# Performance work log

Measured on AMD Instinct MI355X. Metric: run time of the kernel, lower is better.

The kernel has to match this reference:

```python
import jax, jax.numpy as jnp
import numpy as np
from jax import lax

PAD_TOKEN = 1
VOCAB = 32000
HID = 512
B, T, M = 32, 512, 6


def setup_inputs() -> dict:
    key = jax.random.key(0)
    ks = jax.random.split(key, 12)
    lim_g = 1.0 / np.sqrt(HID)
    lim_w = 1.0 / np.sqrt(2 * HID)
    u = lambda k, shape, lim: jax.random.uniform(k, shape, jnp.float32, -lim, lim)
    inp = {
        "input_seqs": jax.random.randint(ks[0], (B, T, M), 0, VOCAB, dtype=jnp.int32),
        "input_lengths": jax.random.randint(ks[1], (B,), 1, T + 1, dtype=jnp.int32),
        "emb": jax.random.normal(ks[2], (VOCAB, HID), jnp.float32),
        # forward GRU cell (Keras GRUCell, reset_after=True)
        "k_f": u(ks[3], (HID, 3 * HID), lim_g),
        "rk_f": u(ks[4], (HID, 3 * HID), lim_g),
        "b_f": u(ks[5], (2, 3 * HID), lim_g),
        # backward GRU cell
        "k_b": u(ks[6], (HID, 3 * HID), lim_g),
        "rk_b": u(ks[7], (HID, 3 * HID), lim_g),
        "b_b": u(ks[8], (2, 3 * HID), lim_g),
        # output projection W: 2H -> H
        "Wk": u(ks[9], (2 * HID, HID), lim_w),
        "Wb": u(ks[10], (HID,), lim_w),
    }
    return inp


def _gru_dir(x, mask, kernel, rkernel, bias, reverse):
    """Masked GRU scan. x: [B,T,H], mask: [B,T] bool. Keras GRUCell (reset_after=True).
    Masked timesteps carry previous state/output through (Keras semantics)."""
    b_in, b_rec = bias[0], bias[1]
    xs = x @ kernel + b_in                      # [B,T,3H], precompute input GEMM
    xs_t = jnp.swapaxes(xs, 0, 1)               # [T,B,3H]
    m_t = jnp.swapaxes(mask, 0, 1)              # [T,B]
    h0 = jnp.zeros((x.shape[0], rkernel.shape[0]), x.dtype)

    def step(h, inp):
        xt, mt = inp
        inner = h @ rkernel + b_rec             # [B,3H]
        xz, xr, xh = jnp.split(xt, 3, axis=-1)
        iz, ir, ih = jnp.split(inner, 3, axis=-1)
        z = jax.nn.sigmoid(xz + iz)
        r = jax.nn.sigmoid(xr + ir)
        hh = jnp.tanh(xh + r * ih)
        hn = z * h + (1.0 - z) * hh
        hn = jnp.where(mt[:, None], hn, h)      # masked step: carry state
        return hn, hn

    hT, outs = lax.scan(step, h0, (xs_t, m_t), reverse=reverse)
    return jnp.swapaxes(outs, 0, 1), hT         # [B,T,H], [B,H]


def reference(input_seqs, input_lengths, emb, k_f, rk_f, b_f, k_b, rk_b, b_b, Wk, Wb):
    # embedding lookup + PAD masking, sum over memory-tuple axis
    e = emb[input_seqs]                                       # [B,T,M,H]
    pad_mask = (input_seqs != PAD_TOKEN).astype(e.dtype)      # [B,T,M]
    embedded = jnp.sum(e * pad_mask[..., None], axis=2)       # [B,T,H]
    # (dropout p=0.0 -> identity)

    time_mask = jnp.arange(T)[None, :] < input_lengths[:, None]  # [B,T] bool

    out_f, h_f = _gru_dir(embedded, time_mask, k_f, rk_f, b_f, reverse=False)
    out_b, h_b = _gru_dir(embedded, time_mask, k_b, rk_b, b_b, reverse=True)

    outputs = jnp.concatenate([out_f, out_b], axis=-1)        # [B,T,2H]
    hidden_hat = jnp.concatenate([h_f, h_b], axis=-1)         # [B,2H]

    hidden = hidden_hat @ Wk + Wb                             # [B,H]
    outputs = outputs @ Wk + Wb                               # [B,T,H]
    return outputs, hidden
```

## Files before the change

kernel.cpp:

```cpp
#include <hip/hip_runtime.h>

typedef _Float16 f16;
typedef f16  f16x8 __attribute__((ext_vector_type(8)));
typedef float f32x4 __attribute__((ext_vector_type(4)));
typedef unsigned int u32;
typedef unsigned long long u64;
typedef u32 u32x4 __attribute__((ext_vector_type(4)));

#define NB   32
#define NT   512
#define NM   6
#define NH   512
#define NH3  1536
#define PADTOK 1
#define LO_SCALE 4096.0f
#define LO_INV   (1.0f/4096.0f)

#define FLAGS_OFF 168165376
#define FLAGS_U32 (2 * (NT + 1) * 32)

__global__ __launch_bounds__(128) void k_embed(const int* __restrict__ seqs,
                                               const float* __restrict__ emb,
                                               f16* __restrict__ Ahi,
                                               f16* __restrict__ Alo,
                                               f16* __restrict__ A2,
                                               u32* __restrict__ flags) {
  int row = blockIdx.x;
  int tid = threadIdx.x;
  if (row < 32) {
    for (int c2 = tid; c2 < 1024; c2 += 128)
      A2[(size_t)(16416 + row) * 1024 + c2] = (f16)0.f;
  }
  if (row < 64) {
    for (int j = row * 128 + tid; j < FLAGS_U32; j += 64 * 128)
      flags[j] = 0u;
  }
  const int* tr = seqs + (size_t)row * NM;
  int c0 = tid * 4;
  float acc0 = 0.f, acc1 = 0.f, acc2 = 0.f, acc3 = 0.f;
  for (int m = 0; m < NM; m++) {
    int tk = tr[m];
    if (tk != PADTOK) {
      float4 ev = *(const float4*)(emb + (size_t)tk * NH + c0);
      acc0 += ev.x; acc1 += ev.y; acc2 += ev.z; acc3 += ev.w;
    }
  }
  float a[4] = {acc0, acc1, acc2, acc3};
  for (int j = 0; j < 4; j++) {
    float v = a[j];
    f16 h = (f16)v;
    float lo = (v - (float)h) * LO_SCALE;
    Ahi[(size_t)row * NH + c0 + j] = h;
    Alo[(size_t)row * NH + c0 + j] = (f16)lo;
  }
}

__global__ __launch_bounds__(256) void k_gemm_in(const f16* __restrict__ Ahi,
                                                 const f16* __restrict__ Alo,
                                                 const float* __restrict__ Bw,
                                                 const float* __restrict__ bias,
                                                 f16* __restrict__ Cxs,
                                                 f16* __restrict__ Clo) {
  __shared__ f16 BsH[64][40];
  __shared__ f16 BsL[64][40];
  int bx = blockIdx.x, by = blockIdx.y;
  int tid = threadIdx.x;
  int w = tid >> 6, l = tid & 63;
  int row0 = bx * 64 + w * 16;
  int col0 = by * 64;
  int arow = row0 + (l & 15);
  int kg = (l >> 4) * 8;
  f32x4 acc[4], accs[4];
  for (int nt = 0; nt < 4; nt++) {
    float bv = bias[col0 + nt * 16 + (l & 15)];
    f32x4 t = {bv, bv, bv, bv};
    acc[nt] = t;
    f32x4 z = {0.f, 0.f, 0.f, 0.f};
    accs[nt] = z;
  }
  for (int kb = 0; kb < NH; kb += 32) {
    __syncthreads();
    for (int idx = tid; idx < 2048; idx += 256) {
      int n = idx & 63, kl = idx >> 6;
      float v = Bw[(size_t)(kb + kl) * NH3 + col0 + n];
      f16 h = (f16)v;
      BsH[n][kl] = h;
      BsL[n][kl] = (f16)((v - (float)h) * LO_SCALE);
    }
    __syncthreads();
    f16x8 ah = *(const f16x8*)(Ahi + (size_t)arow * NH + kb + kg);
    f16x8 al = *(const f16x8*)(Alo + (size_t)arow * NH + kb + kg);
    for (int nt = 0; nt < 4; nt++) {
      f16x8 bh = *(const f16x8*)(&BsH[nt * 16 + (l & 15)][kg]);
      f16x8 bl = *(const f16x8*)(&BsL[nt * 16 + (l & 15)][kg]);
      acc[nt]  = __builtin_amdgcn_mfma_f32_16x16x32_f16(ah, bh, acc[nt], 0, 0, 0);
      accs[nt] = __builtin_amdgcn_mfma_f32_16x16x32_f16(al, bh, accs[nt], 0, 0, 0);
      accs[nt] = __builtin_amdgcn_mfma_f32_16x16x32_f16(ah, bl, accs[nt], 0, 0, 0);
    }
  }
  for (int nt = 0; nt < 4; nt++)
    for (int r = 0; r < 4; r++) {
      int grow = row0 + (l >> 4) * 4 + r;
      int gcol = col0 + nt * 16 + (l & 15);
      int pr = (grow & (NT - 1)) * 32 + (grow >> 9);
      float v = acc[nt][r] + accs[nt][r] * LO_INV;
      f16 h = (f16)v;
      Cxs[(size_t)pr * NH3 + gcol] = h;
      if (gcol >= 2 * NH)
        Clo[(size_t)pr * NH + (gcol - 2 * NH)] = (f16)(v - (float)h);
    }
}

__global__ __launch_bounds__(128) void k_recur(const f16* __restrict__ xs_f,
                                               const f16* __restrict__ xs_b,
                                               const f16* __restrict__ xhlo_f,
                                               const f16* __restrict__ xhlo_b,
                                               const float* __restrict__ rk_f,
                                               const float* __restrict__ rk_b,
                                               const float* __restrict__ b_f,
                                               const float* __restrict__ b_b,
                                               const int* __restrict__ lens,
                                               u32* __restrict__ hb32,
                                               f16* __restrict__ A2,
                                               u32* __restrict__ flags) {
  __shared__ f16 WsH[48 * 512];
  __shared__ f16 WsL[48 * 512];
  int wg = blockIdx.x;
  int d = wg >> 5;
  int s = wg & 31;
  int u0 = s * 16;
  int tid = threadIdx.x;
  int w = tid >> 6, l = tid & 63;
  const f16*   xs = d ? xs_b : xs_f;
  const f16*   xlo = d ? xhlo_b : xhlo_f;
  const float* rk = d ? rk_b : rk_f;
  const float* bb = d ? b_b  : b_f;

  for (int idx = tid; idx < 48 * 512; idx += 128) {
    int k = idx / 48, n = idx % 48;
    int gcol = (n >> 4) * NH + u0 + (n & 15);
    float v = rk[(size_t)k * NH3 + gcol];
    f16 h = (f16)v;
    f16 lo = (f16)((v - (float)h) * LO_SCALE);
    int byte = (n * 1024 + k * 2) ^ ((n & 7) << 4);
    *(f16*)((char*)WsH + byte) = h;
    *(f16*)((char*)WsL + byte) = lo;
  }
  __syncthreads();

  int c = l & 15;
  float brz = bb[NH3 + 0 * NH + u0 + c];
  float brr = bb[NH3 + 1 * NH + u0 + c];
  float brh = bb[NH3 + 2 * NH + u0 + c];
  int mrow[4], lenv[4];
  float hstate[4];
  int wi_h[4];
  for (int r = 0; r < 4; r++) {
    int b = w * 16 + (l >> 4) * 4 + r;
    mrow[r] = b;
    lenv[r] = lens[b];
    hstate[r] = 0.f;
    wi_h[r] = b * NH + u0 + c;
  }
  const int PLANE = NB * NH;
  for (int r = 0; r < 4; r++)
    __hip_atomic_store(&hb32[(d * 2 + 0) * PLANE + wi_h[r]], 0u,
                       __ATOMIC_RELAXED, __HIP_MEMORY_SCOPE_AGENT);
  asm volatile("s_waitcnt vmcnt(0)" ::: "memory");
  __syncthreads();
  if (tid == 0)
    __hip_atomic_store(&flags[(d * (NT + 1) + 0) * 32 + s], 1u,
                       __ATOMIC_RELAXED, __HIP_MEMORY_SCOPE_AGENT);

  int arow_b = w * 16 + (l & 15);
  int kg = (l >> 4) * 8;
  int cbase = c * 1024;
  int zc = (c & 7) << 4;

#pragma unroll 1
  for (int i = 0; i < NT; i++) {
    int t = d ? (NT - 1 - i) : i;
    int p = i & 1;
    const u32* hrow = hb32 + (size_t)(d * 2 + p) * PLANE + arow_b * NH;
    u32* wplane = hb32 + (size_t)(d * 2 + (p ^ 1)) * PLANE;
    const f16* xrow = xs + (size_t)t * 32 * NH3;
    const f16* xlorow = xlo + (size_t)t * 32 * NH;
    f32x4 a0, a1, a2, s0, s1, s2;
    float xh[4];
    for (int r = 0; r < 4; r++) {
      size_t o = (size_t)mrow[r] * NH3 + u0 + c;
      a0[r] = (float)xrow[o] + brz;
      a1[r] = (float)xrow[o + NH] + brr;
      xh[r] = (float)xrow[o + 2 * NH] + (float)xlorow[(size_t)mrow[r] * NH + u0 + c];
      a2[r] = 0.f; s0[r] = 0.f; s1[r] = 0.f; s2[r] = 0.f;
    }
    if (tid < 32) {
      const u32* fp = flags + (d * (NT + 1) + i) * 32 + tid;
      while (__hip_atomic_load(fp, __ATOMIC_RELAXED, __HIP_MEMORY_SCOPE_AGENT) == 0u)
        __builtin_amdgcn_s_sleep(2);
    }
    __syncthreads();

    u64 q[16][4];
#pragma unroll
    for (int kk = 0; kk < 16; kk++) {
      const u32* fb = hrow + kk * 32 + kg;
#pragma unroll
      for (int j = 0; j < 4; j++)
        q[kk][j] = __hip_atomic_load((const u64*)(fb + 2 * j),
                                     __ATOMIC_RELAXED, __HIP_MEMORY_SCOPE_AGENT);
    }
#pragma unroll
    for (int kk = 0; kk < 16; kk++) {
      union { u32x4 w; f16x8 h; } A, L;
#pragma unroll
      for (int j = 0; j < 4; j++) {
        u32 w0 = (u32)q[kk][j];
        u32 w1 = (u32)(q[kk][j] >> 32);
        A.w[j] = __builtin_amdgcn_perm(w1, w0, 0x05040100u);
        L.w[j] = __builtin_amdgcn_perm(w1, w0, 0x07060302u);
      }
      int kb2 = (kk * 32 + kg) * 2;
      int off = (cbase + kb2) ^ zc;
      f16x8 b0h = *(const f16x8*)((const char*)WsH + off);
      f16x8 b1h = *(const f16x8*)((const char*)WsH + 16384 + off);
      f16x8 b2h = *(const f16x8*)((const char*)WsH + 32768 + off);
      f16x8 b0l = *(const f16x8*)((const char*)WsL + off);
      f16x8 b1l = *(const f16x8*)((const char*)WsL + 16384 + off);
      f16x8 b2l = *(const f16x8*)((const char*)WsL + 32768 + off);
      a0 = __builtin_amdgcn_mfma_f32_16x16x32_f16(A.h, b0h, a0, 0, 0, 0);
      s0 = __builtin_amdgcn_mfma_f32_16x16x32_f16(L.h, b0h, s0, 0, 0, 0);
      s0 = __builtin_amdgcn_mfma_f32_16x16x32_f16(A.h, b0l, s0, 0, 0, 0);
      a1 = __builtin_amdgcn_mfma_f32_16x16x32_f16(A.h, b1h, a1, 0, 0, 0);
      s1 = __builtin_amdgcn_mfma_f32_16x16x32_f16(L.h, b1h, s1, 0, 0, 0);
      s1 = __builtin_amdgcn_mfma_f32_16x16x32_f16(A.h, b1l, s1, 0, 0, 0);
      a2 = __builtin_amdgcn_mfma_f32_16x16x32_f16(A.h, b2h, a2, 0, 0, 0);
      s2 = __builtin_amdgcn_mfma_f32_16x16x32_f16(L.h, b2h, s2, 0, 0, 0);
      s2 = __builtin_amdgcn_mfma_f32_16x16x32_f16(A.h, b2l, s2, 0, 0, 0);
    }

    for (int r = 0; r < 4; r++) {
      float az = a0[r] + s0[r] * LO_INV;
      float ar = a1[r] + s1[r] * LO_INV;
      float ahg = a2[r] + s2[r] * LO_INV;
      float z  = 1.f / (1.f + __expf(-az));
      float rr = 1.f / (1.f + __expf(-ar));
      float hh = tanhf(xh[r] + rr * (ahg + brh));
      float hn = z * hstate[r] + (1.f - z) * hh;
      bool msk = t < lenv[r];
      hn = msk ? hn : hstate[r];
      hstate[r] = hn;
      A2[((size_t)mrow[r] * NT + t) * 1024 + d * NH + u0 + c] = (f16)hn;
      union { f16 f; unsigned short u; } chv, clv;
      chv.f = (f16)hn;
      float lof = (hn - (float)chv.f) * LO_SCALE;
      clv.f = (f16)lof;
      u32 packed = (u32)chv.u | ((u32)clv.u << 16);
      __hip_atomic_store(&wplane[wi_h[r]], packed,
                         __ATOMIC_RELAXED, __HIP_MEMORY_SCOPE_AGENT);
    }
    asm volatile("s_waitcnt vmcnt(0)" ::: "memory");
    __syncthreads();
    if (tid == 0)
      __hip_atomic_store(&flags[(d * (NT + 1) + i + 1) * 32 + s], 1u,
                         __ATOMIC_RELAXED, __HIP_MEMORY_SCOPE_AGENT);
  }
  for (int r = 0; r < 4; r++)
    A2[(size_t)(16384 + mrow[r]) * 1024 + d * NH + u0 + c] = (f16)hstate[r];
}

__global__ __launch_bounds__(256) void k_gemm_out(const f16* __restrict__ A2,
                                                  const float* __restrict__ Wk,
                                                  const float* __restrict__ Wb,
                                                  float* __restrict__ Out) {
  __shared__ f16 Bs[64][40];
  int bx = blockIdx.x, by = blockIdx.y;
  int tid = threadIdx.x;
  int w = tid >> 6, l = tid & 63;
  int row0 = bx * 64 + w * 16;
  int col0 = by * 64;
  int arow = row0 + (l & 15);
  int kg = (l >> 4) * 8;
  f32x4 acc[4];
  for (int nt = 0; nt < 4; nt++) {
    float bv = Wb[col0 + nt * 16 + (l & 15)];
    f32x4 t = {bv, bv, bv, bv};
    acc[nt] = t;
  }
  for (int kb = 0; kb < 1024; kb += 32) {
    __syncthreads();
    for (int idx = tid; idx < 2048; idx += 256) {
      int n = idx & 63, kl = idx >> 6;
      Bs[n][kl] = (f16)Wk[(size_t)(kb + kl) * NH + col0 + n];
    }
    __syncthreads();
    f16x8 av = *(const f16x8*)(A2 + (size_t)arow * 1024 + kb + kg);
    for (int nt = 0; nt < 4; nt++) {
      f16x8 bv = *(const f16x8*)(&Bs[nt * 16 + (l & 15)][kg]);
      acc[nt] = __builtin_amdgcn_mfma_f32_16x16x32_f16(av, bv, acc[nt], 0, 0, 0);
    }
  }
  for (int nt = 0; nt < 4; nt++)
    for (int r = 0; r < 4; r++) {
      int grow = row0 + (l >> 4) * 4 + r;
      if (grow < 16416)
        Out[(size_t)grow * NH + col0 + nt * 16 + (l & 15)] = acc[nt][r];
    }
}

extern "C" void kernel_launch(void* const* d_in, const int* in_sizes, int n_in,
                              void* d_out, int out_size, void* d_ws, size_t ws_size,
                              hipStream_t stream) {
  (void)in_sizes; (void)n_in; (void)out_size; (void)ws_size;
  const int*   seqs = (const int*)d_in[0];
  const int*   lens = (const int*)d_in[1];
  const float* emb  = (const float*)d_in[2];
  const float* k_f  = (const float*)d_in[3];
  const float* rk_f = (const float*)d_in[4];
  const float* b_f  = (const float*)d_in[5];
  const float* k_b  = (const float*)d_in[6];
  const float* rk_b = (const float*)d_in[7];
  const float* b_b  = (const float*)d_in[8];
  const float* Wk   = (const float*)d_in[9];
  const float* Wb   = (const float*)d_in[10];
  float* out = (float*)d_out;
  char* ws = (char*)d_ws;
  f16* A2     = (f16*)(ws + 0);
  f16* Ahi    = (f16*)(ws + 0);
  f16* Alo    = (f16*)(ws + 16777216);
  f16* xs_f   = (f16*)(ws + 33685504);
  f16* xs_b   = (f16*)(ws + 84017152);
  f16* xhlo_f = (f16*)(ws + 134348800);
  f16* xhlo_b = (f16*)(ws + 151126016);
  u32* hb32   = (u32*)(ws + 167903232);
  u32* flags  = (u32*)(ws + FLAGS_OFF);

  hipLaunchKernelGGL(k_embed, dim3(16384), dim3(128), 0, stream, seqs, emb, Ahi, Alo, A2, flags);
  hipLaunchKernelGGL(k_gemm_in, dim3(256, 24), dim3(256), 0, stream, Ahi, Alo, k_f, b_f, xs_f, xhlo_f);
  hipLaunchKernelGGL(k_gemm_in, dim3(256, 24), dim3(256), 0, stream, Ahi, Alo, k_b, b_b, xs_b, xhlo_b);
  hipLaunchKernelGGL(k_recur, dim3(64), dim3(128), 0, stream,
                     xs_f, xs_b, xhlo_f, xhlo_b, rk_f, rk_b, b_f, b_b, lens, hb32, A2, flags);
  hipLaunchKernelGGL(k_gemm_out, dim3(257, 8), dim3(256), 0, stream, A2, Wk, Wb, out);
}
```

Baseline: 4.522 ms.

## Replace per-step flag barrier with step tags embedded in hidden-state words

The recurrence kernel no longer publishes a per-block flag after each timestep and no longer waits on those flags. Instead, a 2-bit step tag goes into the low bits of the low-precision half of each packed hidden-state word. Readers spin on the hidden-state loads themselves, in four groups, until every tag matches the expected step. This removes the store-wait, block barrier and flag write/poll round trip on the serial critical path. In exchange it drops two bits of the lo correction term and adds retry loads while spinning. The A2 output stores also move after the atomic publishes, and the embed kernel now seeds the tag planes instead of clearing flags.

```diff
diff --git a/kernel.cpp b/kernel.cpp
--- a/kernel.cpp
+++ b/kernel.cpp
@@ -16,15 +16,14 @@
 #define LO_SCALE 4096.0f
 #define LO_INV   (1.0f/4096.0f)
 
-#define FLAGS_OFF 168165376
-#define FLAGS_U32 (2 * (NT + 1) * 32)
+#define HB_U32 (2 * 2 * NB * NH)
 
 __global__ __launch_bounds__(128) void k_embed(const int* __restrict__ seqs,
                                                const float* __restrict__ emb,
                                                f16* __restrict__ Ahi,
                                                f16* __restrict__ Alo,
                                                f16* __restrict__ A2,
-                                               u32* __restrict__ flags) {
+                                               u32* __restrict__ hb32) {
   int row = blockIdx.x;
   int tid = threadIdx.x;
   if (row < 32) {
@@ -32,8 +31,10 @@
       A2[(size_t)(16416 + row) * 1024 + c2] = (f16)0.f;
   }
   if (row < 64) {
-    for (int j = row * 128 + tid; j < FLAGS_U32; j += 64 * 128)
-      flags[j] = 0u;
+    for (int j = row * 128 + tid; j < HB_U32; j += 64 * 128) {
+      u32 par = (j >> 14) & 1;
+      hb32[j] = par ? 0x00000000u : 0x00010000u;
+    }
   }
   const int* tr = seqs + (size_t)row * NM;
   int c0 = tid * 4;
@@ -121,8 +122,7 @@
                                                const float* __restrict__ b_b,
                                                const int* __restrict__ lens,
                                                u32* __restrict__ hb32,
-                                               f16* __restrict__ A2,
-                                               u32* __restrict__ flags) {
+                                               f16* __restrict__ A2) {
   __shared__ f16 WsH[48 * 512];
   __shared__ f16 WsL[48 * 512];
   int wg = blockIdx.x;
@@ -166,16 +166,12 @@
   for (int r = 0; r < 4; r++)
     __hip_atomic_store(&hb32[(d * 2 + 0) * PLANE + wi_h[r]], 0u,
                        __ATOMIC_RELAXED, __HIP_MEMORY_SCOPE_AGENT);
-  asm volatile("s_waitcnt vmcnt(0)" ::: "memory");
-  __syncthreads();
-  if (tid == 0)
-    __hip_atomic_store(&flags[(d * (NT + 1) + 0) * 32 + s], 1u,
-                       __ATOMIC_RELAXED, __HIP_MEMORY_SCOPE_AGENT);
 
   int arow_b = w * 16 + (l & 15);
   int kg = (l >> 4) * 8;
   int cbase = c * 1024;
   int zc = (c & 7) << 4;
+  const u64 TAGM = 0x0000000300000003ULL;
 
 #pragma unroll 1
   for (int i = 0; i < NT; i++) {
@@ -183,33 +179,67 @@
     int p = i & 1;
     const u32* hrow = hb32 + (size_t)(d * 2 + p) * PLANE + arow_b * NH;
     u32* wplane = hb32 + (size_t)(d * 2 + (p ^ 1)) * PLANE;
-    const f16* xrow = xs + (size_t)t * 32 * NH3;
-    const f16* xlorow = xlo + (size_t)t * 32 * NH;
+    const unsigned short* xrow = (const unsigned short*)(xs + (size_t)t * 32 * NH3);
+    const unsigned short* xlorow = (const unsigned short*)(xlo + (size_t)t * 32 * NH);
+    unsigned short rxz[4], rxr[4], rxh[4], rxl[4];
+#pragma unroll
+    for (int r = 0; r < 4; r++) {
+      size_t o = (size_t)mrow[r] * NH3 + u0 + c;
+      rxz[r] = xrow[o];
+      rxr[r] = xrow[o + NH];
+      rxh[r] = xrow[o + 2 * NH];
+      rxl[r] = xlorow[(size_t)mrow[r] * NH + u0 + c];
+    }
+
+    u32 want = (u32)i & 3u;
+    u64 wp = (u64)want | ((u64)want << 32);
+    u64 q[16][4];
+    bool nd0 = true, nd1 = true, nd2 = true, nd3 = true;
+    do {
+#pragma unroll
+      for (int g = 0; g < 4; g++) {
+        bool nd = (g == 0) ? nd0 : (g == 1) ? nd1 : (g == 2) ? nd2 : nd3;
+        if (nd) {
+#pragma unroll
+          for (int kk2 = 0; kk2 < 4; kk2++) {
+            int kk = g * 4 + kk2;
+            const u32* fb = hrow + kk * 32 + kg;
+#pragma unroll
+            for (int j = 0; j < 4; j++)
+              q[kk][j] = __hip_atomic_load((const u64*)(fb + 2 * j),
+                                           __ATOMIC_RELAXED, __HIP_MEMORY_SCOPE_AGENT);
+          }
+        }
+      }
+#pragma unroll
+      for (int g = 0; g < 4; g++) {
+        bool nd = (g == 0) ? nd0 : (g == 1) ? nd1 : (g == 2) ? nd2 : nd3;
+        if (nd) {
+          u64 acc = 0;
+#pragma unroll
+          for (int kk2 = 0; kk2 < 4; kk2++)
+#pragma unroll
+            for (int j = 0; j < 4; j++)
+              acc |= ((q[g * 4 + kk2][j] >> 16) ^ wp) & TAGM;
+          bool ok = __all(acc == 0ULL);
+          if (g == 0) nd0 = !ok; else if (g == 1) nd1 = !ok;
+          else if (g == 2) nd2 = !ok; else nd3 = !ok;
+        }
+      }
+    } while (nd0 | nd1 | nd2 | nd3);
+
     f32x4 a0, a1, a2, s0, s1, s2;
     float xh[4];
-    for (int r = 0; r < 4; r++) {
-      size_t o = (size_t)mrow[r] * NH3 + u0 + c;
-      a0[r] = (float)xrow[o] + brz;
-      a1[r] = (float)xrow[o + NH] + brr;
-      xh[r] = (float)xrow[o + 2 * NH] + (float)xlorow[(size_t)mrow[r] * NH + u0 + c];
+#pragma unroll
+    for (int r = 0; r < 4; r++) {
+      union { unsigned short u; f16 f; } uz, ur, uh, ul;
+      uz.u = rxz[r]; ur.u = rxr[r]; uh.u = rxh[r]; ul.u = rxl[r];
+      a0[r] = (float)uz.f + brz;
+      a1[r] = (float)ur.f + brr;
+      xh[r] = (float)uh.f + (float)ul.f;
       a2[r] = 0.f; s0[r] = 0.f; s1[r] = 0.f; s2[r] = 0.f;
     }
-    if (tid < 32) {
-      const u32* fp = flags + (d * (NT + 1) + i) * 32 + tid;
-      while (__hip_atomic_load(fp, __ATOMIC_RELAXED, __HIP_MEMORY_SCOPE_AGENT) == 0u)
-        __builtin_amdgcn_s_sleep(2);
-    }
-    __syncthreads();
-
-    u64 q[16][4];
-#pragma unroll
-    for (int kk = 0; kk < 16; kk++) {
-      const u32* fb = hrow + kk * 32 + kg;
-#pragma unroll
-      for (int j = 0; j < 4; j++)
-        q[kk][j] = __hip_atomic_load((const u64*)(fb + 2 * j),
-                                     __ATOMIC_RELAXED, __HIP_MEMORY_SCOPE_AGENT);
-    }
+
 #pragma unroll
     for (int kk = 0; kk < 16; kk++) {
       union { u32x4 w; f16x8 h; } A, L;
@@ -218,7 +248,7 @@
         u32 w0 = (u32)q[kk][j];
         u32 w1 = (u32)(q[kk][j] >> 32);
         A.w[j] = __builtin_amdgcn_perm(w1, w0, 0x05040100u);
-        L.w[j] = __builtin_amdgcn_perm(w1, w0, 0x07060302u);
+        L.w[j] = __builtin_amdgcn_perm(w1, w0, 0x07060302u) & 0xFFFCFFFCu;
       }
       int kb2 = (kk * 32 + kg) * 2;
       int off = (cbase + kb2) ^ zc;
@@ -239,6 +269,8 @@
       s2 = __builtin_amdgcn_mfma_f32_16x16x32_f16(A.h, b2l, s2, 0, 0, 0);
     }
 
+    u32 wtag = (u32)(i + 1) & 3u;
+#pragma unroll
     for (int r = 0; r < 4; r++) {
       float az = a0[r] + s0[r] * LO_INV;
       float ar = a1[r] + s1[r] * LO_INV;
@@ -250,20 +282,17 @@
       bool msk = t < lenv[r];
       hn = msk ? hn : hstate[r];
       hstate[r] = hn;
-      A2[((size_t)mrow[r] * NT + t) * 1024 + d * NH + u0 + c] = (f16)hn;
       union { f16 f; unsigned short u; } chv, clv;
       chv.f = (f16)hn;
       float lof = (hn - (float)chv.f) * LO_SCALE;
       clv.f = (f16)lof;
-      u32 packed = (u32)chv.u | ((u32)clv.u << 16);
+      u32 packed = (u32)chv.u | ((((u32)clv.u & 0xFFFCu) | wtag) << 16);
       __hip_atomic_store(&wplane[wi_h[r]], packed,
                          __ATOMIC_RELAXED, __HIP_MEMORY_SCOPE_AGENT);
     }
-    asm volatile("s_waitcnt vmcnt(0)" ::: "memory");
-    __syncthreads();
-    if (tid == 0)
-      __hip_atomic_store(&flags[(d * (NT + 1) + i + 1) * 32 + s], 1u,
-                         __ATOMIC_RELAXED, __HIP_MEMORY_SCOPE_AGENT);
+#pragma unroll
+    for (int r = 0; r < 4; r++)
+      A2[((size_t)mrow[r] * NT + t) * 1024 + d * NH + u0 + c] = (f16)hstate[r];
   }
   for (int r = 0; r < 4; r++)
     A2[(size_t)(16384 + mrow[r]) * 1024 + d * NH + u0 + c] = (f16)hstate[r];
@@ -333,12 +362,11 @@
   f16* xhlo_f = (f16*)(ws + 134348800);
   f16* xhlo_b = (f16*)(ws + 151126016);
   u32* hb32   = (u32*)(ws + 167903232);
-  u32* flags  = (u32*)(ws + FLAGS_OFF);
-
-  hipLaunchKernelGGL(k_embed, dim3(16384), dim3(128), 0, stream, seqs, emb, Ahi, Alo, A2, flags);
+
+  hipLaunchKernelGGL(k_embed, dim3(16384), dim3(128), 0, stream, seqs, emb, Ahi, Alo, A2, hb32);
   hipLaunchKernelGGL(k_gemm_in, dim3(256, 24), dim3(256), 0, stream, Ahi, Alo, k_f, b_f, xs_f, xhlo_f);
   hipLaunchKernelGGL(k_gemm_in, dim3(256, 24), dim3(256), 0, stream, Ahi, Alo, k_b, b_b, xs_b, xhlo_b);
   hipLaunchKernelGGL(k_recur, dim3(64), dim3(128), 0, stream,
-                     xs_f, xs_b, xhlo_f, xhlo_b, rk_f, rk_b, b_f, b_b, lens, hb32, A2, flags);
+                     xs_f, xs_b, xhlo_f, xhlo_b, rk_f, rk_b, b_f, b_b, lens, hb32, A2);
   hipLaunchKernelGGL(k_gemm_out, dim3(257, 8), dim3(256), 0, stream, A2, Wk, Wb, out);
 }
```

New measurement: 4.995 ms. +10.5%, slower.

## Shorten GRU step critical path: defer output stores, reorder x loads, relayout flags

Applied to the files above, without the earlier changes.

The x-projection loads now issue after the flag wait and h loads instead of before, so they can overlap with the hidden-state fetch. Their values are added after the MFMAs rather than used to seed the accumulators. The A2 output store moves after the flag publish, so the vmcnt(0) wait before signalling only covers the h-plane stores. Flags are relaid out per producer block with a padded stride, and the spin sleep is shortened, to cut cross-block handoff latency in the recurrent loop. In exchange the flag region grows, and the shorter sleep means more polling traffic.

```diff
diff --git a/kernel.cpp b/kernel.cpp
--- a/kernel.cpp
+++ b/kernel.cpp
@@ -17,7 +17,8 @@
 #define LO_INV   (1.0f/4096.0f)
 
 #define FLAGS_OFF 168165376
-#define FLAGS_U32 (2 * (NT + 1) * 32)
+#define SLOT_STRIDE 544
+#define FLAGS_U32 (2 * 32 * SLOT_STRIDE)
 
 __global__ __launch_bounds__(128) void k_embed(const int* __restrict__ seqs,
                                                const float* __restrict__ emb,
@@ -163,13 +164,14 @@
     wi_h[r] = b * NH + u0 + c;
   }
   const int PLANE = NB * NH;
+  const int fbase = (d * 32 + s) * SLOT_STRIDE;
   for (int r = 0; r < 4; r++)
     __hip_atomic_store(&hb32[(d * 2 + 0) * PLANE + wi_h[r]], 0u,
                        __ATOMIC_RELAXED, __HIP_MEMORY_SCOPE_AGENT);
   asm volatile("s_waitcnt vmcnt(0)" ::: "memory");
   __syncthreads();
   if (tid == 0)
-    __hip_atomic_store(&flags[(d * (NT + 1) + 0) * 32 + s], 1u,
+    __hip_atomic_store(&flags[fbase + 0], 1u,
                        __ATOMIC_RELAXED, __HIP_MEMORY_SCOPE_AGENT);
 
   int arow_b = w * 16 + (l & 15);
@@ -183,21 +185,13 @@
     int p = i & 1;
     const u32* hrow = hb32 + (size_t)(d * 2 + p) * PLANE + arow_b * NH;
     u32* wplane = hb32 + (size_t)(d * 2 + (p ^ 1)) * PLANE;
-    const f16* xrow = xs + (size_t)t * 32 * NH3;
-    const f16* xlorow = xlo + (size_t)t * 32 * NH;
-    f32x4 a0, a1, a2, s0, s1, s2;
-    float xh[4];
-    for (int r = 0; r < 4; r++) {
-      size_t o = (size_t)mrow[r] * NH3 + u0 + c;
-      a0[r] = (float)xrow[o] + brz;
-      a1[r] = (float)xrow[o + NH] + brr;
-      xh[r] = (float)xrow[o + 2 * NH] + (float)xlorow[(size_t)mrow[r] * NH + u0 + c];
-      a2[r] = 0.f; s0[r] = 0.f; s1[r] = 0.f; s2[r] = 0.f;
-    }
+    const unsigned short* xrow = (const unsigned short*)(xs + (size_t)t * 32 * NH3);
+    const unsigned short* xlorow = (const unsigned short*)(xlo + (size_t)t * 32 * NH);
+
     if (tid < 32) {
-      const u32* fp = flags + (d * (NT + 1) + i) * 32 + tid;
+      const u32* fp = flags + (d * 32 + tid) * SLOT_STRIDE + i;
       while (__hip_atomic_load(fp, __ATOMIC_RELAXED, __HIP_MEMORY_SCOPE_AGENT) == 0u)
-        __builtin_amdgcn_s_sleep(2);
+        __builtin_amdgcn_s_sleep(1);
     }
     __syncthreads();
 
@@ -209,6 +203,22 @@
       for (int j = 0; j < 4; j++)
         q[kk][j] = __hip_atomic_load((const u64*)(fb + 2 * j),
                                      __ATOMIC_RELAXED, __HIP_MEMORY_SCOPE_AGENT);
+    }
+    unsigned short rxz[4], rxr[4], rxh[4], rxl[4];
+#pragma unroll
+    for (int r = 0; r < 4; r++) {
+      size_t o = (size_t)mrow[r] * NH3 + u0 + c;
+      rxz[r] = xrow[o];
+      rxr[r] = xrow[o + NH];
+      rxh[r] = xrow[o + 2 * NH];
+      rxl[r] = xlorow[(size_t)mrow[r] * NH + u0 + c];
+    }
+
+    f32x4 a0, a1, a2, s0, s1, s2;
+#pragma unroll
+    for (int r = 0; r < 4; r++) {
+      a0[r] = 0.f; a1[r] = 0.f; a2[r] = 0.f;
+      s0[r] = 0.f; s1[r] = 0.f; s2[r] = 0.f;
     }
 #pragma unroll
     for (int kk = 0; kk < 16; kk++) {
@@ -239,18 +249,21 @@
       s2 = __builtin_amdgcn_mfma_f32_16x16x32_f16(A.h, b2l, s2, 0, 0, 0);
     }
 
-    for (int r = 0; r < 4; r++) {
-      float az = a0[r] + s0[r] * LO_INV;
-      float ar = a1[r] + s1[r] * LO_INV;
+#pragma unroll
+    for (int r = 0; r < 4; r++) {
+      union { unsigned short u; f16 f; } uz, ur, uh, ul;
+      uz.u = rxz[r]; ur.u = rxr[r]; uh.u = rxh[r]; ul.u = rxl[r];
+      float az = a0[r] + s0[r] * LO_INV + (float)uz.f + brz;
+      float ar = a1[r] + s1[r] * LO_INV + (float)ur.f + brr;
       float ahg = a2[r] + s2[r] * LO_INV;
+      float xh = (float)uh.f + (float)ul.f;
       float z  = 1.f / (1.f + __expf(-az));
       float rr = 1.f / (1.f + __expf(-ar));
-      float hh = tanhf(xh[r] + rr * (ahg + brh));
+      float hh = tanhf(xh + rr * (ahg + brh));
       float hn = z * hstate[r] + (1.f - z) * hh;
       bool msk = t < lenv[r];
       hn = msk ? hn : hstate[r];
       hstate[r] = hn;
-      A2[((size_t)mrow[r] * NT + t) * 1024 + d * NH + u0 + c] = (f16)hn;
       union { f16 f; unsigned short u; } chv, clv;
       chv.f = (f16)hn;
       float lof = (hn - (float)chv.f) * LO_SCALE;
@@ -262,8 +275,11 @@
     asm volatile("s_waitcnt vmcnt(0)" ::: "memory");
     __syncthreads();
     if (tid == 0)
-      __hip_atomic_store(&flags[(d * (NT + 1) + i + 1) * 32 + s], 1u,
+      __hip_atomic_store(&flags[fbase + i + 1], 1u,
                          __ATOMIC_RELAXED, __HIP_MEMORY_SCOPE_AGENT);
+#pragma unroll
+    for (int r = 0; r < 4; r++)
+      A2[((size_t)mrow[r] * NT + t) * 1024 + d * NH + u0 + c] = (f16)hstate[r];
   }
   for (int r = 0; r < 4; r++)
     A2[(size_t)(16384 + mrow[r]) * 1024 + d * NH + u0 + c] = (f16)hstate[r];
```

New measurement: 4.569 ms. No clear change (+1.0%).
